# Kernel optimization log

Measured on AMD Instinct MI355X. Metric: run time of the kernel, lower is better.

The kernel has to match this reference:

```python
import jax, jax.numpy as jnp
import numpy as np

N, E = 16384, 262144
N_FEAT, N_DIMS, N_CLSS = 128, 64, 40
SIGMA = 1.0
EPS = 1e-8  # torch cosine_similarity / F.normalize eps


def setup_inputs() -> dict:
    key = jax.random.key(0)
    ks = jax.random.split(key, 12)
    d = {
        'x': jax.random.normal(ks[0], (N, N_FEAT), dtype=jnp.float32),
        'edge_index': jax.random.randint(ks[1], (2, E), 0, N, dtype=jnp.int32),
        # SAGEConv1: lin_l (on aggregated neighbors, has bias), lin_r (on root, no bias)
        'W1l': jax.random.normal(ks[2], (N_FEAT, N_DIMS), dtype=jnp.float32) / np.sqrt(N_FEAT),
        'b1': jnp.zeros((N_DIMS,), dtype=jnp.float32),
        'W1r': jax.random.normal(ks[3], (N_FEAT, N_DIMS), dtype=jnp.float32) / np.sqrt(N_FEAT),
        # SAGEConv2
        'W2l': jax.random.normal(ks[4], (N_DIMS, N_DIMS), dtype=jnp.float32) / np.sqrt(N_DIMS),
        'b2': jnp.zeros((N_DIMS,), dtype=jnp.float32),
        'W2r': jax.random.normal(ks[5], (N_DIMS, N_DIMS), dtype=jnp.float32) / np.sqrt(N_DIMS),
        # aux anchor vector
        'aux': jax.random.normal(ks[6], (N_DIMS,), dtype=jnp.float32),
        # classifier Linear(2*n_dims, n_clss)
        'Wc': jax.random.normal(ks[7], (2 * N_DIMS, N_CLSS), dtype=jnp.float32) / np.sqrt(2 * N_DIMS),
        'bc': jnp.zeros((N_CLSS,), dtype=jnp.float32),
    }
    return d


def _sage_conv(x, src, dst, Wl, Wr, b):
    # PyG SAGEConv with mean aggregation: out = lin_l(mean_{j in N(i)} x_j) + lin_r(x_i)
    msg = x[src]  # [E, d]
    agg = jax.ops.segment_sum(msg, dst, num_segments=N)
    cnt = jax.ops.segment_sum(jnp.ones((src.shape[0],), dtype=x.dtype), dst, num_segments=N)
    agg = agg / jnp.maximum(cnt, 1.0)[:, None]  # isolated nodes -> 0
    return agg @ Wl + b + x @ Wr


def _kernel_aggregate(h, aux):
    a = aux / jnp.maximum(jnp.linalg.norm(aux), EPS)           # F.normalize(aux)
    hn = jnp.maximum(jnp.linalg.norm(h, axis=-1), EPS)         # cosine_similarity denom (||a||=1)
    score = (h @ a) / hn                                       # [N]
    diff = score[None, :] - score[:, None]                     # [N, N]
    kappa = jnp.exp(-(diff * diff) / (SIGMA * SIGMA))          # [N, N]
    z = (kappa @ h) / jnp.sum(kappa, axis=1, keepdims=True)
    return z


def reference(x, edge_index, W1l, b1, W1r, W2l, b2, W2r, aux, Wc, bc):
    src, dst = edge_index[0], edge_index[1]
    h = jax.nn.relu(_sage_conv(x, src, dst, W1l, W1r, b1))
    # dropout: eval mode -> identity
    h = _sage_conv(h, src, dst, W2l, W2r, b2)
    z = _kernel_aggregate(h, aux)
    out = jnp.concatenate([h, z], axis=-1) @ Wc + bc
    return out
```

## Files before the change

kernel.cpp:

```cpp
#include <hip/hip_runtime.h>

#define N_NODES 16384
#define N_EDGES 262144
#define F_IN    128
#define DIM     64
#define N_CLS   40
#define KTERMS  24
#define EPSF    1e-8f

__global__ __launch_bounds__(256) void k_degree(const int* __restrict__ dst,
                                                int* __restrict__ deg) {
    int e = blockIdx.x * 256 + threadIdx.x;
    if (e < N_EDGES) atomicAdd(&deg[dst[e]], 1);
}

__global__ __launch_bounds__(1024) void k_scan(const int* __restrict__ deg,
                                               int* __restrict__ base,
                                               int* __restrict__ offs) {
    const int tid = threadIdx.x, lane = tid & 63, w = tid >> 6;
    int loc[16];
    int s = 0;
    const int b0 = tid * 16;
#pragma unroll
    for (int k = 0; k < 16; ++k) { loc[k] = s; s += deg[b0 + k]; }
    int v = s;
#pragma unroll
    for (int off = 1; off < 64; off <<= 1) {
        int t = __shfl_up(v, off);
        if (lane >= off) v += t;
    }
    __shared__ int wsum[16];
    if (lane == 63) wsum[w] = v;
    __syncthreads();
    if (w == 0 && lane < 16) {
        int x = wsum[lane];
#pragma unroll
        for (int off = 1; off < 16; off <<= 1) {
            int t = __shfl_up(x, off);
            if (lane >= off) x += t;
        }
        wsum[lane] = x;
    }
    __syncthreads();
    const int wbase = (w == 0) ? 0 : wsum[w - 1];
    const int excl  = wbase + v - s;
#pragma unroll
    for (int k = 0; k < 16; ++k) {
        int bb = excl + loc[k];
        base[b0 + k] = bb;
        offs[b0 + k] = bb;
    }
}

__global__ __launch_bounds__(256) void k_bucket(const int* __restrict__ src,
                                                const int* __restrict__ dst,
                                                int* __restrict__ offs,
                                                int* __restrict__ ssrc) {
    int e = blockIdx.x * 256 + threadIdx.x;
    if (e < N_EDGES) {
        int pos = atomicAdd(&offs[dst[e]], 1);
        ssrc[pos] = src[e];
    }
}

template<int KDIM>
__global__ __launch_bounds__(256) void k_proj(const float* __restrict__ X,
                                              const float* __restrict__ Wl,
                                              const float* __restrict__ Wr,
                                              float* __restrict__ p,
                                              float* __restrict__ r) {
    __shared__ float sWl[KDIM * DIM];
    __shared__ float sWr[KDIM * DIM];
    __shared__ float sx[4][4][KDIM];
    const int tid = threadIdx.x, lane = tid & 63, w = tid >> 6;
    for (int idx = tid; idx < KDIM * DIM; idx += 256) {
        sWl[idx] = Wl[idx];
        sWr[idx] = Wr[idx];
    }
    __syncthreads();
    const int nw = gridDim.x * 4;
    for (int g = blockIdx.x * 4 + w; g < N_NODES / 4; g += nw) {
        const int row0 = g * 4;
        const float4* xs = (const float4*)(X + (size_t)row0 * KDIM);
        float4* sd = (float4*)&sx[w][0][0];
#pragma unroll
        for (int idx = lane; idx < KDIM; idx += 64) sd[idx] = xs[idx];
        float accl[4] = {0.f, 0.f, 0.f, 0.f};
        float accr[4] = {0.f, 0.f, 0.f, 0.f};
#pragma unroll 16
        for (int k = 0; k < KDIM; ++k) {
            const float wl = sWl[k * DIM + lane];
            const float wr = sWr[k * DIM + lane];
#pragma unroll
            for (int j = 0; j < 4; ++j) {
                const float xv = sx[w][j][k];
                accl[j] = fmaf(xv, wl, accl[j]);
                accr[j] = fmaf(xv, wr, accr[j]);
            }
        }
#pragma unroll
        for (int j = 0; j < 4; ++j) {
            p[(size_t)(row0 + j) * DIM + lane] = accl[j];
            r[(size_t)(row0 + j) * DIM + lane] = accr[j];
        }
    }
}

__global__ __launch_bounds__(256) void k_gather(const int* __restrict__ ssrc,
                                                const int* __restrict__ base,
                                                const int* __restrict__ deg,
                                                const float* __restrict__ p,
                                                const float* __restrict__ r,
                                                const float* __restrict__ b,
                                                float* __restrict__ h, int relu) {
    const int lane = threadIdx.x & 63, w = threadIdx.x >> 6;
    const int node = blockIdx.x * 4 + w;
    if (node >= N_NODES) return;
    const int s0 = base[node];
    const int d  = deg[node];
    float acc = 0.f;
    for (int j0 = 0; j0 < d; j0 += 64) {
        const int m  = min(64, d - j0);
        const int eid = (lane < m) ? ssrc[s0 + j0 + lane] : 0;
        for (int t = 0; t < m; ++t) {
            const int s = __shfl(eid, t);
            acc += p[(size_t)s * DIM + lane];
        }
    }
    float v = acc / fmaxf((float)d, 1.0f) + b[lane] + r[(size_t)node * DIM + lane];
    if (relu) v = fmaxf(v, 0.0f);
    h[(size_t)node * DIM + lane] = v;
}

__global__ __launch_bounds__(256) void k_moments(const float* __restrict__ h,
                                                 const float* __restrict__ aux,
                                                 float* __restrict__ score,
                                                 float* __restrict__ Mm) {
    const int lane = threadIdx.x & 63;
    const int wid  = threadIdx.x >> 6;
    const int gw   = blockIdx.x * 4 + wid;
    const int nw   = gridDim.x * 4;

    float a   = aux[lane];
    float an2 = a * a;
#pragma unroll
    for (int off = 32; off >= 1; off >>= 1) an2 += __shfl_xor(an2, off);
    const float anorm = fmaxf(sqrtf(an2), EPSF);

    float accM[KTERMS], accm[KTERMS];
#pragma unroll
    for (int k = 0; k < KTERMS; ++k) { accM[k] = 0.f; accm[k] = 0.f; }

    for (int i = gw; i < N_NODES; i += nw) {
        float hv = h[(size_t)i * DIM + lane];
        float d1 = hv * a, d2 = hv * hv;
#pragma unroll
        for (int off = 32; off >= 1; off >>= 1) {
            d1 += __shfl_xor(d1, off);
            d2 += __shfl_xor(d2, off);
        }
        float s = d1 / (anorm * fmaxf(sqrtf(d2), EPSF));
        if (lane == 0) score[i] = s;
        float t = expf(-s * s);
#pragma unroll
        for (int k = 0; k < KTERMS; ++k) {
            accM[k] = fmaf(t, hv, accM[k]);
            accm[k] += t;
            t *= s;
        }
    }

    __shared__ float sM[KTERMS][DIM];
    __shared__ float sm[KTERMS];
    if (wid == 0) {
#pragma unroll
        for (int k = 0; k < KTERMS; ++k) sM[k][lane] = accM[k];
        if (lane == 0)
            for (int k = 0; k < KTERMS; ++k) sm[k] = accm[k];
    }
    __syncthreads();
    if (wid != 0) {
        for (int k = 0; k < KTERMS; ++k) atomicAdd(&sM[k][lane], accM[k]);
        if (lane == 0)
            for (int k = 0; k < KTERMS; ++k) atomicAdd(&sm[k], accm[k]);
    }
    __syncthreads();
    if (wid == 0) {
        for (int k = 0; k < KTERMS; ++k) atomicAdd(&Mm[k * DIM + lane], sM[k][lane]);
        if (lane < KTERMS) atomicAdd(&Mm[KTERMS * DIM + lane], sm[lane]);
    }
}

__global__ __launch_bounds__(256) void k_zcls(const float* __restrict__ score,
                                              const float* __restrict__ Mm,
                                              const float* __restrict__ h,
                                              const float* __restrict__ Wc,
                                              const float* __restrict__ bc,
                                              float* __restrict__ out) {
    __shared__ float sM[KTERMS * DIM];
    __shared__ float sm[KTERMS];
    __shared__ float sW[2 * DIM * N_CLS];
    __shared__ float sb[N_CLS];
    __shared__ float sh[4][DIM];
    __shared__ float sz[4][DIM];
    const int tid = threadIdx.x;
    for (int idx = tid; idx < KTERMS * DIM; idx += 256) sM[idx] = Mm[idx];
    if (tid < KTERMS) sm[tid] = Mm[KTERMS * DIM + tid];
    for (int idx = tid; idx < 2 * DIM * N_CLS; idx += 256) sW[idx] = Wc[idx];
    if (tid < N_CLS) sb[tid] = bc[tid];
    __syncthreads();

    const int lane = tid & 63, w = tid >> 6;
    const int gw = blockIdx.x * 4 + w, nw = gridDim.x * 4;
    for (int i = gw; i < N_NODES; i += nw) {
        const float s2 = 2.f * score[i];
        float c = 1.f, num = 0.f, den = 0.f;
#pragma unroll
        for (int k = 0; k < KTERMS; ++k) {
            num = fmaf(c, sM[k * DIM + lane], num);
            den = fmaf(c, sm[k], den);
            c *= s2 * (1.0f / (float)(k + 1));
        }
        sz[w][lane] = num / den;
        sh[w][lane] = h[(size_t)i * DIM + lane];
        if (lane < N_CLS) {
            float acc = sb[lane];
#pragma unroll 8
            for (int k = 0; k < DIM; ++k)
                acc = fmaf(sh[w][k], sW[k * N_CLS + lane], acc);
#pragma unroll 8
            for (int k = 0; k < DIM; ++k)
                acc = fmaf(sz[w][k], sW[(DIM + k) * N_CLS + lane], acc);
            out[(size_t)i * N_CLS + lane] = acc;
        }
    }
}

extern "C" void kernel_launch(void* const* d_in, const int* in_sizes, int n_in,
                              void* d_out, int out_size, void* d_ws, size_t ws_size,
                              hipStream_t stream) {
    const float* x   = (const float*)d_in[0];
    const int*   ei  = (const int*)d_in[1];
    const float* W1l = (const float*)d_in[2];
    const float* b1  = (const float*)d_in[3];
    const float* W1r = (const float*)d_in[4];
    const float* W2l = (const float*)d_in[5];
    const float* b2  = (const float*)d_in[6];
    const float* W2r = (const float*)d_in[7];
    const float* aux = (const float*)d_in[8];
    const float* Wc  = (const float*)d_in[9];
    const float* bc  = (const float*)d_in[10];
    float*       out = (float*)d_out;

    const int* src = ei;
    const int* dst = ei + N_EDGES;

    float*       W  = (float*)d_ws;
    const size_t ND = (size_t)N_NODES * DIM;
    float* pp    = W;
    float* rr    = W + ND;
    float* h1    = W + 2 * ND;
    float* hh    = W + 3 * ND;
    float* score = W + 4 * ND;
    int*   deg   = (int*)(score + N_NODES);
    float* Mm    = (float*)(deg + N_NODES);
    int*   base  = (int*)(Mm + KTERMS * (DIM + 1));
    int*   offs  = base + N_NODES;
    int*   ssrc  = offs + N_NODES;

    hipMemsetAsync(deg, 0, (N_NODES + KTERMS * (DIM + 1)) * sizeof(float), stream);

    k_degree<<<N_EDGES / 256, 256, 0, stream>>>(dst, deg);
    k_scan<<<1, 1024, 0, stream>>>(deg, base, offs);
    k_bucket<<<N_EDGES / 256, 256, 0, stream>>>(src, dst, offs, ssrc);

    k_proj<F_IN><<<512, 256, 0, stream>>>(x, W1l, W1r, pp, rr);
    k_gather<<<N_NODES / 4, 256, 0, stream>>>(ssrc, base, deg, pp, rr, b1, h1, 1);

    k_proj<DIM><<<512, 256, 0, stream>>>(h1, W2l, W2r, pp, rr);
    k_gather<<<N_NODES / 4, 256, 0, stream>>>(ssrc, base, deg, pp, rr, b2, hh, 0);

    k_moments<<<256, 256, 0, stream>>>(hh, aux, score, Mm);
    k_zcls<<<1024, 256, 0, stream>>>(score, Mm, hh, Wc, bc, out);
}
```

Baseline: 229.8 us.

## Fuse neighbor gather with projection and moments into two SAGE kernels

Replaces the separate projection and gather kernels with two fused kernels. Each one gathers neighbor features, averages them, and applies both weight matrices from shared memory. The second also computes scores and moment accumulation, which removes the separate moments kernel and the intermediate p/r buffers. The zeroing of Mm moves into the scan kernel, shrinking the memset. The trade-off is that layer 1 now gathers 128-wide input rows instead of 64-wide projected rows, which doubles that layer's gather traffic.

```diff
diff --git a/kernel.cpp b/kernel.cpp
--- a/kernel.cpp
+++ b/kernel.cpp
@@ -16,7 +16,10 @@
 
 __global__ __launch_bounds__(1024) void k_scan(const int* __restrict__ deg,
                                                int* __restrict__ base,
-                                               int* __restrict__ offs) {
+                                               int* __restrict__ offs,
+                                               float* __restrict__ Mm) {
+    for (int i = threadIdx.x; i < KTERMS * (DIM + 1); i += 1024) Mm[i] = 0.f;
+
     const int tid = threadIdx.x, lane = tid & 63, w = tid >> 6;
     int loc[16];
     int s = 0;
@@ -63,86 +66,107 @@
     }
 }
 
-template<int KDIM>
-__global__ __launch_bounds__(256) void k_proj(const float* __restrict__ X,
-                                              const float* __restrict__ Wl,
-                                              const float* __restrict__ Wr,
-                                              float* __restrict__ p,
-                                              float* __restrict__ r) {
-    __shared__ float sWl[KDIM * DIM];
-    __shared__ float sWr[KDIM * DIM];
-    __shared__ float sx[4][4][KDIM];
+__global__ __launch_bounds__(256) void k_sage1(const int* __restrict__ ssrc,
+                                               const int* __restrict__ base,
+                                               const int* __restrict__ deg,
+                                               const float* __restrict__ x,
+                                               const float* __restrict__ W1l,
+                                               const float* __restrict__ W1r,
+                                               const float* __restrict__ b1,
+                                               float* __restrict__ h1) {
+    __shared__ float sWl[F_IN * DIM];
+    __shared__ float sWr[F_IN * DIM];
+    __shared__ float sag[4][4][F_IN];
+    __shared__ float sxr[4][4][F_IN];
     const int tid = threadIdx.x, lane = tid & 63, w = tid >> 6;
-    for (int idx = tid; idx < KDIM * DIM; idx += 256) {
-        sWl[idx] = Wl[idx];
-        sWr[idx] = Wr[idx];
-    }
-    __syncthreads();
+
+    const float4* wl4 = (const float4*)W1l;
+    const float4* wr4 = (const float4*)W1r;
+    float4* swl4 = (float4*)sWl;
+    float4* swr4 = (float4*)sWr;
+    for (int i = tid; i < F_IN * DIM / 4; i += 256) { swl4[i] = wl4[i]; swr4[i] = wr4[i]; }
+    __syncthreads();
+
+    const float bb = b1[lane];
     const int nw = gridDim.x * 4;
     for (int g = blockIdx.x * 4 + w; g < N_NODES / 4; g += nw) {
-        const int row0 = g * 4;
-        const float4* xs = (const float4*)(X + (size_t)row0 * KDIM);
-        float4* sd = (float4*)&sx[w][0][0];
-#pragma unroll
-        for (int idx = lane; idx < KDIM; idx += 64) sd[idx] = xs[idx];
+#pragma unroll
+        for (int jj = 0; jj < 4; ++jj) {
+            const int node = g * 4 + jj;
+            const int s0 = base[node], d = deg[node];
+            float2 acc = make_float2(0.f, 0.f);
+            for (int j0 = 0; j0 < d; j0 += 64) {
+                const int m = min(64, d - j0);
+                const int eid = (lane < m) ? ssrc[s0 + j0 + lane] : 0;
+                int t = 0;
+                for (; t + 8 <= m; t += 8) {
+                    float2 v[8];
+#pragma unroll
+                    for (int u = 0; u < 8; ++u) {
+                        int s = __shfl(eid, t + u);
+                        v[u] = ((const float2*)(x + (size_t)s * F_IN))[lane];
+                    }
+#pragma unroll
+                    for (int u = 0; u < 8; ++u) { acc.x += v[u].x; acc.y += v[u].y; }
+                }
+                for (; t < m; ++t) {
+                    int s = __shfl(eid, t);
+                    float2 v = ((const float2*)(x + (size_t)s * F_IN))[lane];
+                    acc.x += v.x; acc.y += v.y;
+                }
+            }
+            const float inv = 1.f / fmaxf((float)d, 1.f);
+            acc.x *= inv; acc.y *= inv;
+            ((float2*)sag[w][jj])[lane] = acc;
+            ((float2*)sxr[w][jj])[lane] = ((const float2*)(x + (size_t)node * F_IN))[lane];
+        }
         float accl[4] = {0.f, 0.f, 0.f, 0.f};
         float accr[4] = {0.f, 0.f, 0.f, 0.f};
-#pragma unroll 16
-        for (int k = 0; k < KDIM; ++k) {
-            const float wl = sWl[k * DIM + lane];
-            const float wr = sWr[k * DIM + lane];
-#pragma unroll
-            for (int j = 0; j < 4; ++j) {
-                const float xv = sx[w][j][k];
-                accl[j] = fmaf(xv, wl, accl[j]);
-                accr[j] = fmaf(xv, wr, accr[j]);
-            }
-        }
-#pragma unroll
-        for (int j = 0; j < 4; ++j) {
-            p[(size_t)(row0 + j) * DIM + lane] = accl[j];
-            r[(size_t)(row0 + j) * DIM + lane] = accr[j];
-        }
-    }
-}
-
-__global__ __launch_bounds__(256) void k_gather(const int* __restrict__ ssrc,
-                                                const int* __restrict__ base,
-                                                const int* __restrict__ deg,
-                                                const float* __restrict__ p,
-                                                const float* __restrict__ r,
-                                                const float* __restrict__ b,
-                                                float* __restrict__ h, int relu) {
-    const int lane = threadIdx.x & 63, w = threadIdx.x >> 6;
-    const int node = blockIdx.x * 4 + w;
-    if (node >= N_NODES) return;
-    const int s0 = base[node];
-    const int d  = deg[node];
-    float acc = 0.f;
-    for (int j0 = 0; j0 < d; j0 += 64) {
-        const int m  = min(64, d - j0);
-        const int eid = (lane < m) ? ssrc[s0 + j0 + lane] : 0;
-        for (int t = 0; t < m; ++t) {
-            const int s = __shfl(eid, t);
-            acc += p[(size_t)s * DIM + lane];
-        }
-    }
-    float v = acc / fmaxf((float)d, 1.0f) + b[lane] + r[(size_t)node * DIM + lane];
-    if (relu) v = fmaxf(v, 0.0f);
-    h[(size_t)node * DIM + lane] = v;
-}
-
-__global__ __launch_bounds__(256) void k_moments(const float* __restrict__ h,
-                                                 const float* __restrict__ aux,
-                                                 float* __restrict__ score,
-                                                 float* __restrict__ Mm) {
-    const int lane = threadIdx.x & 63;
-    const int wid  = threadIdx.x >> 6;
-    const int gw   = blockIdx.x * 4 + wid;
-    const int nw   = gridDim.x * 4;
-
-    float a   = aux[lane];
-    float an2 = a * a;
+#pragma unroll 8
+        for (int k = 0; k < F_IN; ++k) {
+            const float wlv = sWl[k * DIM + lane];
+            const float wrv = sWr[k * DIM + lane];
+#pragma unroll
+            for (int jj = 0; jj < 4; ++jj) {
+                accl[jj] = fmaf(sag[w][jj][k], wlv, accl[jj]);
+                accr[jj] = fmaf(sxr[w][jj][k], wrv, accr[jj]);
+            }
+        }
+#pragma unroll
+        for (int jj = 0; jj < 4; ++jj)
+            h1[(size_t)(g * 4 + jj) * DIM + lane] = fmaxf(accl[jj] + accr[jj] + bb, 0.f);
+    }
+}
+
+__global__ __launch_bounds__(256) void k_sage2(const int* __restrict__ ssrc,
+                                               const int* __restrict__ base,
+                                               const int* __restrict__ deg,
+                                               const float* __restrict__ h1,
+                                               const float* __restrict__ W2l,
+                                               const float* __restrict__ W2r,
+                                               const float* __restrict__ b2,
+                                               const float* __restrict__ aux,
+                                               float* __restrict__ h2,
+                                               float* __restrict__ score,
+                                               float* __restrict__ Mm) {
+    __shared__ float sWl[DIM * DIM];
+    __shared__ float sWr[DIM * DIM];
+    __shared__ float sag[4][4][DIM];
+    __shared__ float shr[4][4][DIM];
+    __shared__ float sM[KTERMS][DIM];
+    __shared__ float smm[KTERMS];
+    const int tid = threadIdx.x, lane = tid & 63, w = tid >> 6;
+
+    const float4* wl4 = (const float4*)W2l;
+    const float4* wr4 = (const float4*)W2r;
+    float4* swl4 = (float4*)sWl;
+    float4* swr4 = (float4*)sWr;
+    for (int i = tid; i < DIM * DIM / 4; i += 256) { swl4[i] = wl4[i]; swr4[i] = wr4[i]; }
+    __syncthreads();
+
+    const float bb = b2[lane];
+    const float av = aux[lane];
+    float an2 = av * av;
 #pragma unroll
     for (int off = 32; off >= 1; off >>= 1) an2 += __shfl_xor(an2, off);
     const float anorm = fmaxf(sqrtf(an2), EPSF);
@@ -151,43 +175,87 @@
 #pragma unroll
     for (int k = 0; k < KTERMS; ++k) { accM[k] = 0.f; accm[k] = 0.f; }
 
-    for (int i = gw; i < N_NODES; i += nw) {
-        float hv = h[(size_t)i * DIM + lane];
-        float d1 = hv * a, d2 = hv * hv;
-#pragma unroll
-        for (int off = 32; off >= 1; off >>= 1) {
-            d1 += __shfl_xor(d1, off);
-            d2 += __shfl_xor(d2, off);
-        }
-        float s = d1 / (anorm * fmaxf(sqrtf(d2), EPSF));
-        if (lane == 0) score[i] = s;
-        float t = expf(-s * s);
-#pragma unroll
-        for (int k = 0; k < KTERMS; ++k) {
-            accM[k] = fmaf(t, hv, accM[k]);
-            accm[k] += t;
-            t *= s;
-        }
-    }
-
-    __shared__ float sM[KTERMS][DIM];
-    __shared__ float sm[KTERMS];
-    if (wid == 0) {
+    const int nw = gridDim.x * 4;
+    for (int g = blockIdx.x * 4 + w; g < N_NODES / 4; g += nw) {
+#pragma unroll
+        for (int jj = 0; jj < 4; ++jj) {
+            const int node = g * 4 + jj;
+            const int s0 = base[node], d = deg[node];
+            float acc = 0.f;
+            for (int j0 = 0; j0 < d; j0 += 64) {
+                const int m = min(64, d - j0);
+                const int eid = (lane < m) ? ssrc[s0 + j0 + lane] : 0;
+                int t = 0;
+                for (; t + 8 <= m; t += 8) {
+                    float v[8];
+#pragma unroll
+                    for (int u = 0; u < 8; ++u) {
+                        int s = __shfl(eid, t + u);
+                        v[u] = h1[(size_t)s * DIM + lane];
+                    }
+#pragma unroll
+                    for (int u = 0; u < 8; ++u) acc += v[u];
+                }
+                for (; t < m; ++t) {
+                    int s = __shfl(eid, t);
+                    acc += h1[(size_t)s * DIM + lane];
+                }
+            }
+            sag[w][jj][lane] = acc / fmaxf((float)d, 1.f);
+            shr[w][jj][lane] = h1[(size_t)node * DIM + lane];
+        }
+        float accl[4] = {0.f, 0.f, 0.f, 0.f};
+        float accr[4] = {0.f, 0.f, 0.f, 0.f};
+#pragma unroll 8
+        for (int k = 0; k < DIM; ++k) {
+            const float wlv = sWl[k * DIM + lane];
+            const float wrv = sWr[k * DIM + lane];
+#pragma unroll
+            for (int jj = 0; jj < 4; ++jj) {
+                accl[jj] = fmaf(sag[w][jj][k], wlv, accl[jj]);
+                accr[jj] = fmaf(shr[w][jj][k], wrv, accr[jj]);
+            }
+        }
+#pragma unroll
+        for (int jj = 0; jj < 4; ++jj) {
+            const int node = g * 4 + jj;
+            const float hv = accl[jj] + accr[jj] + bb;
+            h2[(size_t)node * DIM + lane] = hv;
+            float d1 = hv * av, d2 = hv * hv;
+#pragma unroll
+            for (int off = 32; off >= 1; off >>= 1) {
+                d1 += __shfl_xor(d1, off);
+                d2 += __shfl_xor(d2, off);
+            }
+            const float s = d1 / (anorm * fmaxf(sqrtf(d2), EPSF));
+            if (lane == 0) score[node] = s;
+            float t = expf(-s * s);
+#pragma unroll
+            for (int k = 0; k < KTERMS; ++k) {
+                accM[k] = fmaf(t, hv, accM[k]);
+                accm[k] += t;
+                t *= s;
+            }
+        }
+    }
+
+    __syncthreads();
+    if (w == 0) {
 #pragma unroll
         for (int k = 0; k < KTERMS; ++k) sM[k][lane] = accM[k];
         if (lane == 0)
-            for (int k = 0; k < KTERMS; ++k) sm[k] = accm[k];
-    }
-    __syncthreads();
-    if (wid != 0) {
+            for (int k = 0; k < KTERMS; ++k) smm[k] = accm[k];
+    }
+    __syncthreads();
+    if (w != 0) {
         for (int k = 0; k < KTERMS; ++k) atomicAdd(&sM[k][lane], accM[k]);
         if (lane == 0)
-            for (int k = 0; k < KTERMS; ++k) atomicAdd(&sm[k], accm[k]);
-    }
-    __syncthreads();
-    if (wid == 0) {
+            for (int k = 0; k < KTERMS; ++k) atomicAdd(&smm[k], accm[k]);
+    }
+    __syncthreads();
+    if (w == 0) {
         for (int k = 0; k < KTERMS; ++k) atomicAdd(&Mm[k * DIM + lane], sM[k][lane]);
-        if (lane < KTERMS) atomicAdd(&Mm[KTERMS * DIM + lane], sm[lane]);
+        if (lane < KTERMS) atomicAdd(&Mm[KTERMS * DIM + lane], smm[lane]);
     }
 }
 
@@ -257,29 +325,21 @@
 
     float*       W  = (float*)d_ws;
     const size_t ND = (size_t)N_NODES * DIM;
-    float* pp    = W;
-    float* rr    = W + ND;
-    float* h1    = W + 2 * ND;
-    float* hh    = W + 3 * ND;
-    float* score = W + 4 * ND;
+    float* h1    = W;
+    float* hh    = W + ND;
+    float* score = W + 2 * ND;
     int*   deg   = (int*)(score + N_NODES);
     float* Mm    = (float*)(deg + N_NODES);
     int*   base  = (int*)(Mm + KTERMS * (DIM + 1));
     int*   offs  = base + N_NODES;
     int*   ssrc  = offs + N_NODES;
 
-    hipMemsetAsync(deg, 0, (N_NODES + KTERMS * (DIM + 1)) * sizeof(float), stream);
-
+    hipMemsetAsync(deg, 0, N_NODES * sizeof(int), stream);
     k_degree<<<N_EDGES / 256, 256, 0, stream>>>(dst, deg);
-    k_scan<<<1, 1024, 0, stream>>>(deg, base, offs);
+    k_scan<<<1, 1024, 0, stream>>>(deg, base, offs, Mm);
     k_bucket<<<N_EDGES / 256, 256, 0, stream>>>(src, dst, offs, ssrc);
 
-    k_proj<F_IN><<<512, 256, 0, stream>>>(x, W1l, W1r, pp, rr);
-    k_gather<<<N_NODES / 4, 256, 0, stream>>>(ssrc, base, deg, pp, rr, b1, h1, 1);
-
-    k_proj<DIM><<<512, 256, 0, stream>>>(h1, W2l, W2r, pp, rr);
-    k_gather<<<N_NODES / 4, 256, 0, stream>>>(ssrc, base, deg, pp, rr, b2, hh, 0);
-
-    k_moments<<<256, 256, 0, stream>>>(hh, aux, score, Mm);
-    k_zcls<<<1024, 256, 0, stream>>>(score, Mm, hh, Wc, bc, out);
-}
+    k_sage1<<<512, 256, 0, stream>>>(ssrc, base, deg, x, W1l, W1r, b1, h1);
+    k_sage2<<<512, 256, 0, stream>>>(ssrc, base, deg, h1, W2l, W2r, b2, aux, hh, score, Mm);
+    k_zcls<<<512, 256, 0, stream>>>(score, Mm, hh, Wc, bc, out);
+}
```

Result: no change. 233.6 us (+1.7%).
